# Kernel optimization log

Hardware: AMD Instinct MI355X
Metric: run time of the kernel (lower is better)

The kernel has to match this reference:

```python
import jax, jax.numpy as jnp
import numpy as np

B, T, C, H, W = 2, 8, 512, 32, 32
HEADS, HD = 8, 64          # head_dim = C // num_heads
GROUPS = 32                # GroupNorm_0 num_groups
EPS = 1e-6


def setup_inputs() -> dict:
    key = jax.random.key(0)
    k = jax.random.split(key, 5)
    return {
        "x": jax.random.normal(k[0], (B, T, C, H, W), jnp.float32),
        "gn_scale": jnp.ones((C,), jnp.float32),
        "gn_bias": jnp.zeros((C,), jnp.float32),
        "w_qkv": jax.random.normal(k[1], (C, 3 * C), jnp.float32) / float(np.sqrt(C)),
        "b_qkv": jnp.zeros((3 * C,), jnp.float32),
        "w_out": jax.random.normal(k[2], (C, C), jnp.float32) / float(np.sqrt(C)),
        "b_out": jnp.zeros((C,), jnp.float32),
    }


def reference(x, gn_scale, gn_bias, w_qkv, b_qkv, w_out, b_out):
    Bv, Tv, Cv, Hv, Wv = x.shape
    N = Bv * Tv
    xv = x.reshape(N, Cv, Hv, Wv)

    # GroupNorm(32 groups, eps=1e-6) with affine
    g = xv.reshape(N, GROUPS, Cv // GROUPS, Hv, Wv)
    mu = g.mean(axis=(2, 3, 4), keepdims=True)
    var = g.var(axis=(2, 3, 4), keepdims=True)
    hn = ((g - mu) * jax.lax.rsqrt(var + EPS)).reshape(N, Cv, Hv, Wv)
    hn = hn * gn_scale[None, :, None, None] + gn_bias[None, :, None, None]

    # NIN qkv projection (per-pixel 1x1): (N,C,H,W) x (C,3C) -> (N,3C,H,W)
    h = jnp.einsum('nchw,cd->ndhw', hn, w_qkv) + b_qkv[None, :, None, None]
    h = h.reshape(N, HEADS, 3 * HD, Hv * Wv).transpose(0, 1, 3, 2)  # (N,h,S,3d)
    q, k, v = jnp.split(h, 3, axis=-1)

    # naive scaled dot-product attention over S = H*W tokens
    logits = jnp.einsum('nhsd,nhtd->nhst', q, k) / float(np.sqrt(HD))
    attn = jax.nn.softmax(logits, axis=-1)
    vals = jnp.einsum('nhst,nhtd->nhsd', attn, v)

    h = vals.transpose(0, 1, 3, 2).reshape(N, Cv, Hv, Wv)
    # output NIN (init_scale=0 in torch; random params here) + residual
    h = jnp.einsum('nchw,cd->ndhw', h, w_out) + b_out[None, :, None, None]
    return x + h.reshape(Bv, Tv, Cv, Hv, Wv)
```

## Files before the change

kernel.cpp:

```cpp
#include <hip/hip_runtime.h>
#include <stdint.h>

typedef __bf16 bf16x8 __attribute__((ext_vector_type(8)));
typedef float f32x4v __attribute__((ext_vector_type(4)));
typedef float f32x16v __attribute__((ext_vector_type(16)));
typedef unsigned u32x2 __attribute__((ext_vector_type(2)));

__device__ __forceinline__ unsigned f2bf_rn(float f) {
    return (__float_as_uint(f) + 0x8000u) >> 16;
}
__device__ __forceinline__ unsigned pk2bf(float a, float b) {
    return __builtin_amdgcn_perm(__float_as_uint(b) + 0x8000u,
                                 __float_as_uint(a) + 0x8000u, 0x07060302u);
}
__device__ __forceinline__ unsigned pk2bf_rne(float a, float b) {
    union { __bf16 h[2]; unsigned u; } x;
    x.h[0] = (__bf16)a; x.h[1] = (__bf16)b;
    return x.u;
}
__device__ __forceinline__ float fexp2(float x) {
#if __has_builtin(__builtin_amdgcn_exp2f)
    return __builtin_amdgcn_exp2f(x);
#else
    float r; asm volatile("v_exp_f32 %0, %1" : "=v"(r) : "v"(x)); return r;
#endif
}
__device__ __forceinline__ float frcp(float x) {
#if __has_builtin(__builtin_amdgcn_rcpf)
    return __builtin_amdgcn_rcpf(x);
#else
    float r; asm volatile("v_rcp_f32 %0, %1" : "=v"(r) : "v"(x)); return r;
#endif
}

__device__ __forceinline__ void swap32(unsigned &a, unsigned &b) {
#if __has_builtin(__builtin_amdgcn_permlane32_swap)
    u32x2 r = __builtin_amdgcn_permlane32_swap(a, b, false, false);
    a = r[0]; b = r[1];
#else
    unsigned pa = (unsigned)__shfl_xor((int)a, 32);
    unsigned pb = (unsigned)__shfl_xor((int)b, 32);
    bool hi = (threadIdx.x & 32) != 0;
    unsigned na = hi ? pb : a;
    unsigned nb = hi ? b : pa;
    a = na; b = nb;
#endif
}

__device__ __forceinline__ bf16x8 mk8(unsigned a, unsigned b, unsigned c, unsigned e) {
    union { int4 i; bf16x8 v; } u;
    u.i = make_int4((int)a, (int)b, (int)c, (int)e);
    return u.v;
}

#define GLD_LDS16(gp, lp) __builtin_amdgcn_global_load_lds( \
    (const __attribute__((address_space(1))) unsigned int*)(gp), \
    (__attribute__((address_space(3))) unsigned int*)(lp), 16, 0, 0)

__global__ __launch_bounds__(256) void wt_kernel(const float* __restrict__ wqkv,
        const float* __restrict__ wout, unsigned short* __restrict__ WqT,
        unsigned short* __restrict__ WoT) {
    __shared__ float tile[32][33];
    int bx = blockIdx.x;
    const float* in; unsigned short* out; int Cc, c0;
    if (bx < 48) { in = wqkv; out = WqT; Cc = 1536; c0 = bx * 32; }
    else         { in = wout; out = WoT; Cc = 512;  c0 = (bx - 48) * 32; }
    int r0 = blockIdx.y * 32;
    int tx = threadIdx.x & 31, ty = threadIdx.x >> 5;
    #pragma unroll
    for (int i = 0; i < 4; i++) {
        int r = ty + i * 8;
        tile[r][tx] = in[(size_t)(r0 + r) * Cc + c0 + tx];
    }
    __syncthreads();
    #pragma unroll
    for (int i = 0; i < 4; i++) {
        int cr = ty + i * 8;
        out[(size_t)(c0 + cr) * 512 + r0 + tx] = (unsigned short)f2bf_rn(tile[tx][cr]);
    }
}

__global__ __launch_bounds__(256) void gn_kernel(const float* __restrict__ x,
        const float* __restrict__ scale, const float* __restrict__ bias,
        unsigned short* __restrict__ hnT) {
    int blk = blockIdx.x;
    int tid = threadIdx.x;
    int g = blk & 31, n = blk >> 5;
    const float4* src4 = (const float4*)(x + (size_t)blk * 16384);

    __shared__ float xs[16][1028];
    float s = 0.f, s2 = 0.f;
    #pragma unroll
    for (int k = 0; k < 16; k++) {
        int i = tid + k * 256;
        float4 v = src4[i];
        int c = i >> 8, p4 = (i & 255) * 4;
        *(float4*)&xs[c][p4] = v;
        s  += v.x + v.y + v.z + v.w;
        s2 += v.x*v.x + v.y*v.y + v.z*v.z + v.w*v.w;
    }
    __shared__ float red[256], red2[256];
    red[tid] = s; red2[tid] = s2;
    __syncthreads();
    for (int off = 128; off > 0; off >>= 1) {
        if (tid < off) { red[tid] += red[tid+off]; red2[tid] += red2[tid+off]; }
        __syncthreads();
    }
    __shared__ float sc_s[16], bi_s[16];
    if (tid < 16) {
        float mean = red[0] * (1.f/16384.f);
        float var  = red2[0] * (1.f/16384.f) - mean*mean;
        float rstd = rsqrtf(var + 1e-6f);
        int c = g*16 + tid;
        float sc = scale[c] * rstd;
        sc_s[tid] = sc;
        bi_s[tid] = bias[c] - mean * sc;
    }
    __syncthreads();
    #pragma unroll
    for (int ch = 0; ch < 4; ch++) {
        int sQ = ch*256 + tid;
        unsigned int pk[8];
        #pragma unroll
        for (int c2 = 0; c2 < 8; c2++) {
            float a = xs[c2*2][sQ]   * sc_s[c2*2]   + bi_s[c2*2];
            float b = xs[c2*2+1][sQ] * sc_s[c2*2+1] + bi_s[c2*2+1];
            pk[c2] = pk2bf(a, b);
        }
        unsigned short* op = hnT + ((size_t)(n*1024 + sQ))*512 + g*16;
        *(uint4*)op       = make_uint4(pk[0], pk[1], pk[2], pk[3]);
        *((uint4*)op + 1) = make_uint4(pk[4], pk[5], pk[6], pk[7]);
    }
}

__global__ __launch_bounds__(256) void qkv_kernel(
        const unsigned short* __restrict__ WqT, const unsigned short* __restrict__ hnT,
        const float* __restrict__ bqkv,
        unsigned short* __restrict__ qb, unsigned short* __restrict__ kbuf,
        unsigned short* __restrict__ vb) {
    int s0 = blockIdx.x * 128, m0 = blockIdx.y * 128, n = blockIdx.z;
    __shared__ unsigned short At[8192];
    __shared__ unsigned short Bt[8192];
    int tid = threadIdx.x;
    int lane = tid & 63, w = tid >> 6;
    int quad = lane >> 4, tx = lane & 15;
    int moff = (w & 1) * 64, soff = (w >> 1) * 64;

    const unsigned short* Arow = WqT + (size_t)m0 * 512;
    const unsigned short* Brow = hnT + ((size_t)n * 1024 + s0) * 512;

    f32x4v acc[4][4];
    #pragma unroll
    for (int i = 0; i < 4; i++)
        #pragma unroll
        for (int j = 0; j < 4; j++)
            #pragma unroll
            for (int e = 0; e < 4; e++) acc[i][j][e] = 0.f;

    int f1 = tid, f2 = tid + 256;
    int m1 = f1 >> 2, kb1 = ((f1 & 3) - (f1 >> 3)) & 3;
    int m2 = f2 >> 2, kb2 = ((f2 & 3) - (f2 >> 3)) & 3;

    for (int k0 = 0; k0 < 512; k0 += 64) {
        __syncthreads();
        GLD_LDS16(Arow + (size_t)m1*512 + k0 + kb1*8,      At + f1*8);
        GLD_LDS16(Arow + (size_t)m2*512 + k0 + kb2*8,      At + f2*8);
        GLD_LDS16(Arow + (size_t)m1*512 + k0 + 32 + kb1*8, At + 4096 + f1*8);
        GLD_LDS16(Arow + (size_t)m2*512 + k0 + 32 + kb2*8, At + 4096 + f2*8);
        GLD_LDS16(Brow + (size_t)m1*512 + k0 + kb1*8,      Bt + f1*8);
        GLD_LDS16(Brow + (size_t)m2*512 + k0 + kb2*8,      Bt + f2*8);
        GLD_LDS16(Brow + (size_t)m1*512 + k0 + 32 + kb1*8, Bt + 4096 + f1*8);
        GLD_LDS16(Brow + (size_t)m2*512 + k0 + 32 + kb2*8, Bt + 4096 + f2*8);
        __syncthreads();
        #pragma unroll
        for (int kk = 0; kk < 2; kk++) {
            const unsigned short* Ab = At + kk*4096;
            const unsigned short* Bb = Bt + kk*4096;
            bf16x8 af[4], bfr[4];
            #pragma unroll
            for (int mt = 0; mt < 4; mt++) {
                int m = moff + mt*16 + tx;
                int ch = m*4 + ((quad + (m >> 1)) & 3);
                af[mt] = *(const bf16x8*)(Ab + ch*8);
            }
            #pragma unroll
            for (int nt = 0; nt < 4; nt++) {
                int m = soff + nt*16 + tx;
                int ch = m*4 + ((quad + (m >> 1)) & 3);
                bfr[nt] = *(const bf16x8*)(Bb + ch*8);
            }
            #pragma unroll
            for (int mt = 0; mt < 4; mt++)
                #pragma unroll
                for (int nt = 0; nt < 4; nt++)
                    acc[mt][nt] = __builtin_amdgcn_mfma_f32_16x16x32_bf16(
                        af[mt], bfr[nt], acc[mt][nt], 0, 0, 0);
        }
    }

    const float QSCL = 0.18033688011112042f;
    #pragma unroll
    for (int mt = 0; mt < 4; mt++) {
        int m = m0 + moff + mt*16 + quad*4;
        int head = m / 192;
        int r = m - head*192;
        int which = r >> 6;
        int d0 = r & 63;
        float4 bia = *(const float4*)(bqkv + m);
        float scl = (which == 0) ? QSCL : 1.0f;
        #pragma unroll
        for (int nt = 0; nt < 4; nt++) {
            int sQ = s0 + soff + nt*16 + tx;
            f32x4v a = acc[mt][nt];
            float v0 = (a[0]+bia.x)*scl, v1 = (a[1]+bia.y)*scl;
            float v2 = (a[2]+bia.z)*scl, v3 = (a[3]+bia.w)*scl;
            if (which < 2) {
                unsigned short* base = (which == 0) ? qb : kbuf;
                unsigned lo = pk2bf(v0, v1), hi2 = pk2bf(v2, v3);
                *(uint2*)(base + (((size_t)(n*8 + head)*1024 + sQ) << 6) + d0) =
                    make_uint2(lo, hi2);
            } else {
                size_t vbase = ((size_t)(n*8 + head)*64 + d0)*1024 + sQ;
                vb[vbase]        = (unsigned short)f2bf_rn(v0);
                vb[vbase + 1024] = (unsigned short)f2bf_rn(v1);
                vb[vbase + 2048] = (unsigned short)f2bf_rn(v2);
                vb[vbase + 3072] = (unsigned short)f2bf_rn(v3);
            }
        }
    }
}

__global__ __launch_bounds__(256, 2) void attn_kernel(
        const unsigned short* __restrict__ qg, const unsigned short* __restrict__ kg,
        const unsigned short* __restrict__ vg, unsigned short* __restrict__ ao) {
    int bid = blockIdx.x;
    int nh = bid & 127, qbk = bid >> 7;
    int tid = threadIdx.x, w = tid >> 6, lane = tid & 63;
    int lq = lane & 31, hi = lane >> 5;
    const unsigned short* Q = qg + (size_t)nh * 65536;
    const unsigned short* K = kg + (size_t)nh * 65536;
    const unsigned short* V = vg + (size_t)nh * 65536;

    __shared__ unsigned short Klds[2][64*72];
    __shared__ unsigned short Vlds[2][64*72];

    int q0 = qbk*256 + w*64;
    bf16x8 qfA[4], qfB[4];
    #pragma unroll
    for (int ks = 0; ks < 4; ks++) {
        qfA[ks] = *(const bf16x8*)(Q + ((size_t)(q0 + lq))*64 + ks*16 + hi*8);
        qfB[ks] = *(const bf16x8*)(Q + ((size_t)(q0 + 32 + lq))*64 + ks*16 + hi*8);
    }

    int r = tid >> 2, part = (tid & 3) * 16;
    uint4 ka, kb2, va, vb2;
    ka  = *(const uint4*)(K + (size_t)r*64 + part);
    kb2 = *(const uint4*)(K + (size_t)r*64 + part + 8);
    va  = *(const uint4*)(V + (size_t)r*1024 + part);
    vb2 = *(const uint4*)(V + (size_t)r*1024 + part + 8);

    const bf16x8 ONES = mk8(0x3f803f80u, 0x3f803f80u, 0x3f803f80u, 0x3f803f80u);

    f32x16v O0a, O1a, O0b, O1b, Osa, Osb, ZED;
    #pragma unroll
    for (int i = 0; i < 16; i++) {
        O0a[i] = 0.f; O1a[i] = 0.f; O0b[i] = 0.f; O1b[i] = 0.f;
        Osa[i] = 0.f; Osb[i] = 0.f; ZED[i] = 0.f;
    }

    for (int it = 0; it < 16; it++) {
        int buf = it & 1;
        {
            unsigned short* kd = Klds[buf] + r*72 + part;
            *(uint4*)kd = ka; *(uint4*)(kd+8) = kb2;
            unsigned short* vd = Vlds[buf] + r*72 + part;
            *(uint4*)vd = va; *(uint4*)(vd+8) = vb2;
        }
        __syncthreads();
        if (it < 15) {
            int t0 = (it + 1) * 64;
            ka  = *(const uint4*)(K + (size_t)(t0 + r)*64 + part);
            kb2 = *(const uint4*)(K + (size_t)(t0 + r)*64 + part + 8);
            va  = *(const uint4*)(V + (size_t)r*1024 + t0 + part);
            vb2 = *(const uint4*)(V + (size_t)r*1024 + t0 + part + 8);
        }
        const unsigned short* Kb = Klds[buf];
        const unsigned short* Vb = Vlds[buf];

        f32x16v S0, S1, U0, U1;
        __builtin_amdgcn_s_setprio(1);
        {
            bf16x8 a0 = *(const bf16x8*)(Kb + lq*72 + hi*8);
            bf16x8 a1 = *(const bf16x8*)(Kb + (32+lq)*72 + hi*8);
            S0 = __builtin_amdgcn_mfma_f32_32x32x16_bf16(a0, qfA[0], ZED, 0, 0, 0);
            S1 = __builtin_amdgcn_mfma_f32_32x32x16_bf16(a1, qfA[0], ZED, 0, 0, 0);
            U0 = __builtin_amdgcn_mfma_f32_32x32x16_bf16(a0, qfB[0], ZED, 0, 0, 0);
            U1 = __builtin_amdgcn_mfma_f32_32x32x16_bf16(a1, qfB[0], ZED, 0, 0, 0);
        }
        #pragma unroll
        for (int ks = 1; ks < 4; ks++) {
            bf16x8 a0 = *(const bf16x8*)(Kb + lq*72 + ks*16 + hi*8);
            bf16x8 a1 = *(const bf16x8*)(Kb + (32+lq)*72 + ks*16 + hi*8);
            S0 = __builtin_amdgcn_mfma_f32_32x32x16_bf16(a0, qfA[ks], S0, 0, 0, 0);
            S1 = __builtin_amdgcn_mfma_f32_32x32x16_bf16(a1, qfA[ks], S1, 0, 0, 0);
            U0 = __builtin_amdgcn_mfma_f32_32x32x16_bf16(a0, qfB[ks], U0, 0, 0, 0);
            U1 = __builtin_amdgcn_mfma_f32_32x32x16_bf16(a1, qfB[ks], U1, 0, 0, 0);
        }
        __builtin_amdgcn_s_setprio(0);

        #pragma unroll
        for (int i = 0; i < 16; i++) {
            S0[i] = fexp2(S0[i]);
            S1[i] = fexp2(S1[i]);
        }
        unsigned dA[16];
        #pragma unroll
        for (int p2 = 0; p2 < 8; p2++) {
            dA[p2]     = pk2bf_rne(S0[p2*2], S0[p2*2+1]);
            dA[8 + p2] = pk2bf_rne(S1[p2*2], S1[p2*2+1]);
        }
        swap32(dA[0],  dA[2]);  swap32(dA[1],  dA[3]);
        swap32(dA[4],  dA[6]);  swap32(dA[5],  dA[7]);
        swap32(dA[8],  dA[10]); swap32(dA[9],  dA[11]);
        swap32(dA[12], dA[14]); swap32(dA[13], dA[15]);

        unsigned dB[16];
        {
            bf16x8 paA = mk8(dA[0], dA[1], dA[2], dA[3]);
            bf16x8 v0 = *(const bf16x8*)(Vb + lq*72 + hi*8);
            bf16x8 v1 = *(const bf16x8*)(Vb + (32+lq)*72 + hi*8);
            O0a = __builtin_amdgcn_mfma_f32_32x32x16_bf16(paA, v0, O0a, 0, 0, 0);
            O1a = __builtin_amdgcn_mfma_f32_32x32x16_bf16(paA, v1, O1a, 0, 0, 0);
            Osa = __builtin_amdgcn_mfma_f32_32x32x16_bf16(paA, ONES, Osa, 0, 0, 0);
        }
        #pragma unroll
        for (int i = 0; i < 16; i++) U0[i] = fexp2(U0[i]);
        {
            bf16x8 paA = mk8(dA[4], dA[5], dA[6], dA[7]);
            bf16x8 v0 = *(const bf16x8*)(Vb + lq*72 + 16 + hi*8);
            bf16x8 v1 = *(const bf16x8*)(Vb + (32+lq)*72 + 16 + hi*8);
            O0a = __builtin_amdgcn_mfma_f32_32x32x16_bf16(paA, v0, O0a, 0, 0, 0);
            O1a = __builtin_amdgcn_mfma_f32_32x32x16_bf16(paA, v1, O1a, 0, 0, 0);
            Osa = __builtin_amdgcn_mfma_f32_32x32x16_bf16(paA, ONES, Osa, 0, 0, 0);
        }
        #pragma unroll
        for (int i = 0; i < 16; i++) U1[i] = fexp2(U1[i]);
        {
            bf16x8 paA = mk8(dA[8], dA[9], dA[10], dA[11]);
            bf16x8 v0 = *(const bf16x8*)(Vb + lq*72 + 32 + hi*8);
            bf16x8 v1 = *(const bf16x8*)(Vb + (32+lq)*72 + 32 + hi*8);
            O0a = __builtin_amdgcn_mfma_f32_32x32x16_bf16(paA, v0, O0a, 0, 0, 0);
            O1a = __builtin_amdgcn_mfma_f32_32x32x16_bf16(paA, v1, O1a, 0, 0, 0);
            Osa = __builtin_amdgcn_mfma_f32_32x32x16_bf16(paA, ONES, Osa, 0, 0, 0);
        }
        #pragma unroll
        for (int p2 = 0; p2 < 8; p2++) {
            dB[p2]     = pk2bf_rne(U0[p2*2], U0[p2*2+1]);
            dB[8 + p2] = pk2bf_rne(U1[p2*2], U1[p2*2+1]);
        }
        {
            bf16x8 paA = mk8(dA[12], dA[13], dA[14], dA[15]);
            bf16x8 v0 = *(const bf16x8*)(Vb + lq*72 + 48 + hi*8);
            bf16x8 v1 = *(const bf16x8*)(Vb + (32+lq)*72 + 48 + hi*8);
            O0a = __builtin_amdgcn_mfma_f32_32x32x16_bf16(paA, v0, O0a, 0, 0, 0);
            O1a = __builtin_amdgcn_mfma_f32_32x32x16_bf16(paA, v1, O1a, 0, 0, 0);
            Osa = __builtin_amdgcn_mfma_f32_32x32x16_bf16(paA, ONES, Osa, 0, 0, 0);
        }
        swap32(dB[0],  dB[2]);  swap32(dB[1],  dB[3]);
        swap32(dB[4],  dB[6]);  swap32(dB[5],  dB[7]);
        swap32(dB[8],  dB[10]); swap32(dB[9],  dB[11]);
        swap32(dB[12], dB[14]); swap32(dB[13], dB[15]);

        __builtin_amdgcn_s_setprio(1);
        #pragma unroll
        for (int kc = 0; kc < 4; kc++) {
            bf16x8 paB = mk8(dB[kc*4+0], dB[kc*4+1], dB[kc*4+2], dB[kc*4+3]);
            bf16x8 v0 = *(const bf16x8*)(Vb + lq*72 + kc*16 + hi*8);
            bf16x8 v1 = *(const bf16x8*)(Vb + (32+lq)*72 + kc*16 + hi*8);
            O0b = __builtin_amdgcn_mfma_f32_32x32x16_bf16(paB, v0, O0b, 0, 0, 0);
            O1b = __builtin_amdgcn_mfma_f32_32x32x16_bf16(paB, v1, O1b, 0, 0, 0);
            Osb = __builtin_amdgcn_mfma_f32_32x32x16_bf16(paB, ONES, Osb, 0, 0, 0);
        }
        __builtin_amdgcn_s_setprio(0);
    }

    int n = nh >> 3, h = nh & 7;
    #pragma unroll
    for (int rq = 0; rq < 4; rq++) {
        #pragma unroll
        for (int i = 0; i < 4; i++) {
            int reg = rq*4 + i;
            int sQ = q0 + rq*8 + hi*4 + i;
            float invA = frcp(Osa[reg]);
            float invB = frcp(Osb[reg]);
            size_t rowbA = ((size_t)(n*1024 + sQ))*512 + h*64;
            size_t rowbB = ((size_t)(n*1024 + sQ + 32))*512 + h*64;
            ao[rowbA + lq]      = (unsigned short)f2bf_rn(O0a[reg] * invA);
            ao[rowbA + 32 + lq] = (unsigned short)f2bf_rn(O1a[reg] * invA);
            ao[rowbB + lq]      = (unsigned short)f2bf_rn(O0b[reg] * invB);
            ao[rowbB + 32 + lq] = (unsigned short)f2bf_rn(O1b[reg] * invB);
        }
    }
}

__global__ __launch_bounds__(256) void out_kernel(
        const unsigned short* __restrict__ aoT, const unsigned short* __restrict__ WoT,
        const float* __restrict__ bout, const float* __restrict__ x,
        float* __restrict__ out) {
    int s0 = blockIdx.x * 128, d0b = blockIdx.y * 128, n = blockIdx.z;
    __shared__ unsigned short At[8192];
    __shared__ unsigned short Bt[8192];
    int tid = threadIdx.x;
    int lane = tid & 63, w = tid >> 6;
    int quad = lane >> 4, tx = lane & 15;
    int moff = (w & 1) * 64, noff = (w >> 1) * 64;

    const unsigned short* Arow = aoT + ((size_t)n * 1024 + s0) * 512;
    const unsigned short* Brow = WoT + (size_t)d0b * 512;

    f32x4v acc[4][4];
    #pragma unroll
    for (int i = 0; i < 4; i++)
        #pragma unroll
        for (int j = 0; j < 4; j++)
            #pragma unroll
            for (int e = 0; e < 4; e++) acc[i][j][e] = 0.f;

    int f1 = tid, f2 = tid + 256;
    int m1 = f1 >> 2, kb1 = ((f1 & 3) - (f1 >> 3)) & 3;
    int m2 = f2 >> 2, kb2 = ((f2 & 3) - (f2 >> 3)) & 3;

    for (int k0 = 0; k0 < 512; k0 += 64) {
        __syncthreads();
        GLD_LDS16(Arow + (size_t)m1*512 + k0 + kb1*8,      At + f1*8);
        GLD_LDS16(Arow + (size_t)m2*512 + k0 + kb2*8,      At + f2*8);
        GLD_LDS16(Arow + (size_t)m1*512 + k0 + 32 + kb1*8, At + 4096 + f1*8);
        GLD_LDS16(Arow + (size_t)m2*512 + k0 + 32 + kb2*8, At + 4096 + f2*8);
        GLD_LDS16(Brow + (size_t)m1*512 + k0 + kb1*8,      Bt + f1*8);
        GLD_LDS16(Brow + (size_t)m2*512 + k0 + kb2*8,      Bt + f2*8);
        GLD_LDS16(Brow + (size_t)m1*512 + k0 + 32 + kb1*8, Bt + 4096 + f1*8);
        GLD_LDS16(Brow + (size_t)m2*512 + k0 + 32 + kb2*8, Bt + 4096 + f2*8);
        __syncthreads();
        #pragma unroll
        for (int kk = 0; kk < 2; kk++) {
            const unsigned short* Ab = At + kk*4096;
            const unsigned short* Bb = Bt + kk*4096;
            bf16x8 af[4], bfr[4];
            #pragma unroll
            for (int mt = 0; mt < 4; mt++) {
                int m = moff + mt*16 + tx;
                int ch = m*4 + ((quad + (m >> 1)) & 3);
                af[mt] = *(const bf16x8*)(Ab + ch*8);
            }
            #pragma unroll
            for (int nt = 0; nt < 4; nt++) {
                int m = noff + nt*16 + tx;
                int ch = m*4 + ((quad + (m >> 1)) & 3);
                bfr[nt] = *(const bf16x8*)(Bb + ch*8);
            }
            #pragma unroll
            for (int mt = 0; mt < 4; mt++)
                #pragma unroll
                for (int nt = 0; nt < 4; nt++)
                    acc[mt][nt] = __builtin_amdgcn_mfma_f32_16x16x32_bf16(
                        af[mt], bfr[nt], acc[mt][nt], 0, 0, 0);
        }
    }

    #pragma unroll
    for (int mt = 0; mt < 4; mt++) {
        int sQ = s0 + moff + mt*16 + quad*4;
        #pragma unroll
        for (int nt = 0; nt < 4; nt++) {
            int d = d0b + noff + nt*16 + tx;
            float bo = bout[d];
            size_t base = ((size_t)n*512 + d)*1024 + sQ;
            float4 xv = *(const float4*)(x + base);
            f32x4v a = acc[mt][nt];
            float4 o = make_float4(a[0]+bo+xv.x, a[1]+bo+xv.y, a[2]+bo+xv.z, a[3]+bo+xv.w);
            *(float4*)(out + base) = o;
        }
    }
}

extern "C" void kernel_launch(void* const* d_in, const int* in_sizes, int n_in,
                              void* d_out, int out_size, void* d_ws, size_t ws_size,
                              hipStream_t stream) {
    const float* x    = (const float*)d_in[0];
    const float* gns  = (const float*)d_in[1];
    const float* gnb  = (const float*)d_in[2];
    const float* wqkv = (const float*)d_in[3];
    const float* bqkv = (const float*)d_in[4];
    const float* wout = (const float*)d_in[5];
    const float* bout = (const float*)d_in[6];
    float* out = (float*)d_out;

    char* p = (char*)d_ws;
    size_t off = 0;
    auto carve = [&](size_t bytes) {
        char* r = p + off;
        off = (off + bytes + 255) & ~(size_t)255;
        return r;
    };
    unsigned short* hnT = (unsigned short*)carve((size_t)16*1024*512*2);
    unsigned short* qb2 = (unsigned short*)carve((size_t)128*1024*64*2);
    unsigned short* kb2 = (unsigned short*)carve((size_t)128*1024*64*2);
    unsigned short* vb2 = (unsigned short*)carve((size_t)128*64*1024*2);
    unsigned short* aoT = (unsigned short*)carve((size_t)16*1024*512*2);
    unsigned short* WqT = (unsigned short*)carve((size_t)1536*512*2);
    unsigned short* WoT = (unsigned short*)carve((size_t)512*512*2);

    wt_kernel<<<dim3(64, 16), 256, 0, stream>>>(wqkv, wout, WqT, WoT);
    gn_kernel<<<dim3(512), 256, 0, stream>>>(x, gns, gnb, hnT);
    qkv_kernel<<<dim3(8, 12, 16), 256, 0, stream>>>(WqT, hnT, bqkv, qb2, kb2, vb2);
    attn_kernel<<<dim3(512), 256, 0, stream>>>(qb2, kb2, vb2, aoT);
    out_kernel<<<dim3(8, 4, 16), 256, 0, stream>>>(aoT, WoT, bout, x, out);
}
```

Measured before the change: 200.9 us.

## Load K/V MFMA fragments directly from global memory, dropping LDS staging

The attention kernel no longer stages K and V tiles through double-buffered shared memory with a block-wide barrier per iteration. Each wave now loads its MFMA operand fragments for K and V straight from global memory (served from L2/L1) at the start of each key tile. This removes the LDS writes, the __syncthreads and the LDS reads. In exchange the four waves each fetch the same K/V data redundantly, and the loads are no longer software-prefetched a tile ahead, so global latency may sit on the critical path.

```diff
diff --git a/kernel.cpp b/kernel.cpp
--- a/kernel.cpp
+++ b/kernel.cpp
@@ -241,9 +241,6 @@
     const unsigned short* K = kg + (size_t)nh * 65536;
     const unsigned short* V = vg + (size_t)nh * 65536;
 
-    __shared__ unsigned short Klds[2][64*72];
-    __shared__ unsigned short Vlds[2][64*72];
-
     int q0 = qbk*256 + w*64;
     bf16x8 qfA[4], qfB[4];
     #pragma unroll
@@ -252,12 +249,10 @@
         qfB[ks] = *(const bf16x8*)(Q + ((size_t)(q0 + 32 + lq))*64 + ks*16 + hi*8);
     }
 
-    int r = tid >> 2, part = (tid & 3) * 16;
-    uint4 ka, kb2, va, vb2;
-    ka  = *(const uint4*)(K + (size_t)r*64 + part);
-    kb2 = *(const uint4*)(K + (size_t)r*64 + part + 8);
-    va  = *(const uint4*)(V + (size_t)r*1024 + part);
-    vb2 = *(const uint4*)(V + (size_t)r*1024 + part + 8);
+    const unsigned short* K0 = K + (size_t)lq*64 + hi*8;
+    const unsigned short* K1 = K + (size_t)(32+lq)*64 + hi*8;
+    const unsigned short* V0 = V + (size_t)lq*1024 + hi*8;
+    const unsigned short* V1 = V + (size_t)(32+lq)*1024 + hi*8;
 
     const bf16x8 ONES = mk8(0x3f803f80u, 0x3f803f80u, 0x3f803f80u, 0x3f803f80u);
 
@@ -269,44 +264,36 @@
     }
 
     for (int it = 0; it < 16; it++) {
-        int buf = it & 1;
-        {
-            unsigned short* kd = Klds[buf] + r*72 + part;
-            *(uint4*)kd = ka; *(uint4*)(kd+8) = kb2;
-            unsigned short* vd = Vlds[buf] + r*72 + part;
-            *(uint4*)vd = va; *(uint4*)(vd+8) = vb2;
-        }
-        __syncthreads();
-        if (it < 15) {
-            int t0 = (it + 1) * 64;
-            ka  = *(const uint4*)(K + (size_t)(t0 + r)*64 + part);
-            kb2 = *(const uint4*)(K + (size_t)(t0 + r)*64 + part + 8);
-            va  = *(const uint4*)(V + (size_t)r*1024 + t0 + part);
-            vb2 = *(const uint4*)(V + (size_t)r*1024 + t0 + part + 8);
-        }
-        const unsigned short* Kb = Klds[buf];
-        const unsigned short* Vb = Vlds[buf];
+        int t0 = it * 64;
+
+        bf16x8 k0[4], k1[4];
+        #pragma unroll
+        for (int ks = 0; ks < 4; ks++) {
+            k0[ks] = *(const bf16x8*)(K0 + (size_t)t0*64 + ks*16);
+            k1[ks] = *(const bf16x8*)(K1 + (size_t)t0*64 + ks*16);
+        }
 
         f32x16v S0, S1, U0, U1;
         __builtin_amdgcn_s_setprio(1);
-        {
-            bf16x8 a0 = *(const bf16x8*)(Kb + lq*72 + hi*8);
-            bf16x8 a1 = *(const bf16x8*)(Kb + (32+lq)*72 + hi*8);
-            S0 = __builtin_amdgcn_mfma_f32_32x32x16_bf16(a0, qfA[0], ZED, 0, 0, 0);
-            S1 = __builtin_amdgcn_mfma_f32_32x32x16_bf16(a1, qfA[0], ZED, 0, 0, 0);
-            U0 = __builtin_amdgcn_mfma_f32_32x32x16_bf16(a0, qfB[0], ZED, 0, 0, 0);
-            U1 = __builtin_amdgcn_mfma_f32_32x32x16_bf16(a1, qfB[0], ZED, 0, 0, 0);
-        }
+        S0 = __builtin_amdgcn_mfma_f32_32x32x16_bf16(k0[0], qfA[0], ZED, 0, 0, 0);
+        S1 = __builtin_amdgcn_mfma_f32_32x32x16_bf16(k1[0], qfA[0], ZED, 0, 0, 0);
+        U0 = __builtin_amdgcn_mfma_f32_32x32x16_bf16(k0[0], qfB[0], ZED, 0, 0, 0);
+        U1 = __builtin_amdgcn_mfma_f32_32x32x16_bf16(k1[0], qfB[0], ZED, 0, 0, 0);
         #pragma unroll
         for (int ks = 1; ks < 4; ks++) {
-            bf16x8 a0 = *(const bf16x8*)(Kb + lq*72 + ks*16 + hi*8);
-            bf16x8 a1 = *(const bf16x8*)(Kb + (32+lq)*72 + ks*16 + hi*8);
-            S0 = __builtin_amdgcn_mfma_f32_32x32x16_bf16(a0, qfA[ks], S0, 0, 0, 0);
-            S1 = __builtin_amdgcn_mfma_f32_32x32x16_bf16(a1, qfA[ks], S1, 0, 0, 0);
-            U0 = __builtin_amdgcn_mfma_f32_32x32x16_bf16(a0, qfB[ks], U0, 0, 0, 0);
-            U1 = __builtin_amdgcn_mfma_f32_32x32x16_bf16(a1, qfB[ks], U1, 0, 0, 0);
+            S0 = __builtin_amdgcn_mfma_f32_32x32x16_bf16(k0[ks], qfA[ks], S0, 0, 0, 0);
+            S1 = __builtin_amdgcn_mfma_f32_32x32x16_bf16(k1[ks], qfA[ks], S1, 0, 0, 0);
+            U0 = __builtin_amdgcn_mfma_f32_32x32x16_bf16(k0[ks], qfB[ks], U0, 0, 0, 0);
+            U1 = __builtin_amdgcn_mfma_f32_32x32x16_bf16(k1[ks], qfB[ks], U1, 0, 0, 0);
         }
         __builtin_amdgcn_s_setprio(0);
+
+        bf16x8 v0f[4], v1f[4];
+        #pragma unroll
+        for (int kc = 0; kc < 4; kc++) {
+            v0f[kc] = *(const bf16x8*)(V0 + t0 + kc*16);
+            v1f[kc] = *(const bf16x8*)(V1 + t0 + kc*16);
+        }
 
         #pragma unroll
         for (int i = 0; i < 16; i++) {
@@ -327,30 +314,24 @@
         unsigned dB[16];
         {
             bf16x8 paA = mk8(dA[0], dA[1], dA[2], dA[3]);
-            bf16x8 v0 = *(const bf16x8*)(Vb + lq*72 + hi*8);
-            bf16x8 v1 = *(const bf16x8*)(Vb + (32+lq)*72 + hi*8);
-            O0a = __builtin_amdgcn_mfma_f32_32x32x16_bf16(paA, v0, O0a, 0, 0, 0);
-            O1a = __builtin_amdgcn_mfma_f32_32x32x16_bf16(paA, v1, O1a, 0, 0, 0);
+            O0a = __builtin_amdgcn_mfma_f32_32x32x16_bf16(paA, v0f[0], O0a, 0, 0, 0);
+            O1a = __builtin_amdgcn_mfma_f32_32x32x16_bf16(paA, v1f[0], O1a, 0, 0, 0);
             Osa = __builtin_amdgcn_mfma_f32_32x32x16_bf16(paA, ONES, Osa, 0, 0, 0);
         }
         #pragma unroll
         for (int i = 0; i < 16; i++) U0[i] = fexp2(U0[i]);
         {
             bf16x8 paA = mk8(dA[4], dA[5], dA[6], dA[7]);
-            bf16x8 v0 = *(const bf16x8*)(Vb + lq*72 + 16 + hi*8);
-            bf16x8 v1 = *(const bf16x8*)(Vb + (32+lq)*72 + 16 + hi*8);
-            O0a = __builtin_amdgcn_mfma_f32_32x32x16_bf16(paA, v0, O0a, 0, 0, 0);
-            O1a = __builtin_amdgcn_mfma_f32_32x32x16_bf16(paA, v1, O1a, 0, 0, 0);
+            O0a = __builtin_amdgcn_mfma_f32_32x32x16_bf16(paA, v0f[1], O0a, 0, 0, 0);
+            O1a = __builtin_amdgcn_mfma_f32_32x32x16_bf16(paA, v1f[1], O1a, 0, 0, 0);
             Osa = __builtin_amdgcn_mfma_f32_32x32x16_bf16(paA, ONES, Osa, 0, 0, 0);
         }
         #pragma unroll
         for (int i = 0; i < 16; i++) U1[i] = fexp2(U1[i]);
         {
             bf16x8 paA = mk8(dA[8], dA[9], dA[10], dA[11]);
-            bf16x8 v0 = *(const bf16x8*)(Vb + lq*72 + 32 + hi*8);
-            bf16x8 v1 = *(const bf16x8*)(Vb + (32+lq)*72 + 32 + hi*8);
-            O0a = __builtin_amdgcn_mfma_f32_32x32x16_bf16(paA, v0, O0a, 0, 0, 0);
-            O1a = __builtin_amdgcn_mfma_f32_32x32x16_bf16(paA, v1, O1a, 0, 0, 0);
+            O0a = __builtin_amdgcn_mfma_f32_32x32x16_bf16(paA, v0f[2], O0a, 0, 0, 0);
+            O1a = __builtin_amdgcn_mfma_f32_32x32x16_bf16(paA, v1f[2], O1a, 0, 0, 0);
             Osa = __builtin_amdgcn_mfma_f32_32x32x16_bf16(paA, ONES, Osa, 0, 0, 0);
         }
         #pragma unroll
@@ -360,10 +341,8 @@
         }
         {
             bf16x8 paA = mk8(dA[12], dA[13], dA[14], dA[15]);
-            bf16x8 v0 = *(const bf16x8*)(Vb + lq*72 + 48 + hi*8);
-            bf16x8 v1 = *(const bf16x8*)(Vb + (32+lq)*72 + 48 + hi*8);
-            O0a = __builtin_amdgcn_mfma_f32_32x32x16_bf16(paA, v0, O0a, 0, 0, 0);
-            O1a = __builtin_amdgcn_mfma_f32_32x32x16_bf16(paA, v1, O1a, 0, 0, 0);
+            O0a = __builtin_amdgcn_mfma_f32_32x32x16_bf16(paA, v0f[3], O0a, 0, 0, 0);
+            O1a = __builtin_amdgcn_mfma_f32_32x32x16_bf16(paA, v1f[3], O1a, 0, 0, 0);
             Osa = __builtin_amdgcn_mfma_f32_32x32x16_bf16(paA, ONES, Osa, 0, 0, 0);
         }
         swap32(dB[0],  dB[2]);  swap32(dB[1],  dB[3]);
@@ -375,10 +354,8 @@
         #pragma unroll
         for (int kc = 0; kc < 4; kc++) {
             bf16x8 paB = mk8(dB[kc*4+0], dB[kc*4+1], dB[kc*4+2], dB[kc*4+3]);
-            bf16x8 v0 = *(const bf16x8*)(Vb + lq*72 + kc*16 + hi*8);
-            bf16x8 v1 = *(const bf16x8*)(Vb + (32+lq)*72 + kc*16 + hi*8);
-            O0b = __builtin_amdgcn_mfma_f32_32x32x16_bf16(paB, v0, O0b, 0, 0, 0);
-            O1b = __builtin_amdgcn_mfma_f32_32x32x16_bf16(paB, v1, O1b, 0, 0, 0);
+            O0b = __builtin_amdgcn_mfma_f32_32x32x16_bf16(paB, v0f[kc], O0b, 0, 0, 0);
+            O1b = __builtin_amdgcn_mfma_f32_32x32x16_bf16(paB, v1f[kc], O1b, 0, 0, 0);
             Osb = __builtin_amdgcn_mfma_f32_32x32x16_bf16(paB, ONES, Osb, 0, 0, 0);
         }
         __builtin_amdgcn_s_setprio(0);
```

Measured after the change: 218.8 us. 1.09x slower.
